# Performance work log

Hardware: AMD Instinct MI355X
Metric: run time of the kernel (lower is better)

## Reference

```python
import jax, jax.numpy as jnp
import numpy as np

NUM_HEADS = 12
WINDOW = 14
GLOBAL_LAYERS = (1,)
N_LAYERS = 2
EPS = 1e-6
PATCH = 16


def layer_norm(x, w, b):
    m = x.mean(-1, keepdims=True)
    v = ((x - m) ** 2).mean(-1, keepdims=True)
    return (x - m) * jax.lax.rsqrt(v + EPS) * w + b


def layer_norm_2d(x, w, b):
    # channels_first LayerNorm over C of [B,C,H,W]
    m = x.mean(1, keepdims=True)
    v = ((x - m) ** 2).mean(1, keepdims=True)
    return (x - m) * jax.lax.rsqrt(v + EPS) * w[None, :, None, None] + b[None, :, None, None]


def get_rel_pos(size, rel_pos):
    # q_size == k_size == size and rel_pos has exactly 2*size-1 rows,
    # so F.interpolate is identity -> direct relative-coordinate lookup.
    coords = jnp.arange(size)
    idx = coords[:, None] - coords[None, :] + (size - 1)  # [size, size]
    return rel_pos[idx]  # [size, size, head_dim]


def attention(x, qkv_w, qkv_b, proj_w, proj_b, rel_h, rel_w):
    B, H, W, C = x.shape
    hd = C // NUM_HEADS
    qkv = x.reshape(B, H * W, C) @ qkv_w.T + qkv_b                       # [B,HW,3C]
    qkv = qkv.reshape(B, H * W, 3, NUM_HEADS, hd).transpose(2, 0, 3, 1, 4)
    qkv = qkv.reshape(3, B * NUM_HEADS, H * W, hd)
    q, k, v = qkv[0], qkv[1], qkv[2]
    attn = jnp.einsum('bqd,bkd->bqk', q * (hd ** -0.5), k)               # [Bn,HW,HW]
    Rh = get_rel_pos(H, rel_h)                                           # [H,H,hd]
    Rw = get_rel_pos(W, rel_w)                                           # [W,W,hd]
    qr = q.reshape(B * NUM_HEADS, H, W, hd)
    rel_h_t = jnp.einsum('bhwc,hkc->bhwk', qr, Rh)                       # [Bn,H,W,H]
    rel_w_t = jnp.einsum('bhwc,wkc->bhwk', qr, Rw)                       # [Bn,H,W,W]
    attn = attn.reshape(B * NUM_HEADS, H, W, H, W)
    attn = attn + rel_h_t[:, :, :, :, None] + rel_w_t[:, :, :, None, :]
    attn = attn.reshape(B * NUM_HEADS, H * W, H * W)
    attn = jax.nn.softmax(attn.astype(jnp.float32), axis=-1).astype(q.dtype)
    out = jnp.einsum('bqk,bkd->bqd', attn, v)
    out = out.reshape(B, NUM_HEADS, H, W, hd).transpose(0, 2, 3, 1, 4).reshape(B, H, W, C)
    return out @ proj_w.T + proj_b


def window_partition(x, ws):
    B, H, W, C = x.shape
    pad_h = (-H) % ws
    pad_w = (-W) % ws
    x = jnp.pad(x, ((0, 0), (0, pad_h), (0, pad_w), (0, 0)))
    Hp, Wp = H + pad_h, W + pad_w
    x = x.reshape(B, Hp // ws, ws, Wp // ws, ws, C).transpose(0, 1, 3, 2, 4, 5)
    return x.reshape(-1, ws, ws, C), (Hp, Wp)


def window_unpartition(win, ws, pad_hw, hw):
    Hp, Wp = pad_hw
    H, W = hw
    C = win.shape[-1]
    B = win.shape[0] // ((Hp // ws) * (Wp // ws))
    x = win.reshape(B, Hp // ws, Wp // ws, ws, ws, C).transpose(0, 1, 3, 2, 4, 5)
    return x.reshape(B, Hp, Wp, C)[:, :H, :W, :]


def _forward(pixel_values, patch_w, patch_b, pos_embed, ln1_w, ln1_b, qkv_w, qkv_b,
             proj_w, proj_b, rel_h0, rel_w0, rel_h1, rel_w1, ln2_w, ln2_b,
             mlp1_w, mlp1_b, mlp2_w, mlp2_b, neck_conv1_w, neck_ln1_w, neck_ln1_b,
             neck_conv2_w, neck_ln2_w, neck_ln2_b):
    # patch embed (16x16 stride-16 conv) -> [B,64,64,768]
    x = jax.lax.conv_general_dilated(pixel_values, patch_w, (PATCH, PATCH), 'VALID',
                                     dimension_numbers=('NCHW', 'OIHW', 'NCHW'))
    x = x.transpose(0, 2, 3, 1) + patch_b
    x = x + pos_embed
    rels = [(rel_h0, rel_w0), (rel_h1, rel_w1)]
    for i in range(N_LAYERS):
        shortcut = x
        h = layer_norm(x, ln1_w[i], ln1_b[i])
        ws = 0 if i in GLOBAL_LAYERS else WINDOW
        if ws > 0:
            H, W = h.shape[1], h.shape[2]
            h, pad_hw = window_partition(h, ws)
        h = attention(h, qkv_w[i], qkv_b[i], proj_w[i], proj_b[i], *rels[i])
        if ws > 0:
            h = window_unpartition(h, ws, pad_hw, (H, W))
        x = shortcut + h
        m = layer_norm(x, ln2_w[i], ln2_b[i])
        m = jax.nn.gelu(m @ mlp1_w[i].T + mlp1_b[i], approximate=False)
        x = x + (m @ mlp2_w[i].T + mlp2_b[i])
    # neck: 1x1 conv -> LN2d -> 3x3 conv -> LN2d (convs have no bias)
    x = x.transpose(0, 3, 1, 2)                                          # [B,C,H,W]
    x = jnp.einsum('bchw,oc->bohw', x, neck_conv1_w[:, :, 0, 0])
    x = layer_norm_2d(x, neck_ln1_w, neck_ln1_b)
    x = jax.lax.conv_general_dilated(x, neck_conv2_w, (1, 1), ((1, 1), (1, 1)),
                                     dimension_numbers=('NCHW', 'OIHW', 'NCHW'))
    x = layer_norm_2d(x, neck_ln2_w, neck_ln2_b)
    return x


def setup_inputs() -> dict:
    ks = iter(jax.random.split(jax.random.key(0), 40))

    def rn(shape, s=0.02):
        return jax.random.normal(next(ks), shape, jnp.float32) * s

    C, NL, MLP, OC = 768, N_LAYERS, 3072, 256
    return {
        'pixel_values': jax.random.normal(next(ks), (1, 3, 1024, 1024), jnp.float32),
        'patch_w': rn((C, 3, PATCH, PATCH)),
        'patch_b': rn((C,)),
        'pos_embed': rn((1, 64, 64, C)),
        'ln1_w': jnp.ones((NL, C)), 'ln1_b': jnp.zeros((NL, C)),
        'qkv_w': rn((NL, 3 * C, C)), 'qkv_b': rn((NL, 3 * C)),
        'proj_w': rn((NL, C, C)), 'proj_b': rn((NL, C)),
        'rel_h0': rn((2 * WINDOW - 1, 64)), 'rel_w0': rn((2 * WINDOW - 1, 64)),
        'rel_h1': rn((2 * 64 - 1, 64)), 'rel_w1': rn((2 * 64 - 1, 64)),
        'ln2_w': jnp.ones((NL, C)), 'ln2_b': jnp.zeros((NL, C)),
        'mlp1_w': rn((NL, MLP, C)), 'mlp1_b': rn((NL, MLP)),
        'mlp2_w': rn((NL, C, MLP)), 'mlp2_b': rn((NL, C)),
        'neck_conv1_w': rn((OC, C, 1, 1)),
        'neck_ln1_w': jnp.ones((OC,)), 'neck_ln1_b': jnp.zeros((OC,)),
        'neck_conv2_w': rn((OC, OC, 3, 3)),
        'neck_ln2_w': jnp.ones((OC,)), 'neck_ln2_b': jnp.zeros((OC,)),
    }


def reference(pixel_values, patch_w, patch_b, pos_embed, ln1_w, ln1_b, qkv_w, qkv_b,
              proj_w, proj_b, rel_h0, rel_w0, rel_h1, rel_w1, ln2_w, ln2_b,
              mlp1_w, mlp1_b, mlp2_w, mlp2_b, neck_conv1_w, neck_ln1_w, neck_ln1_b,
              neck_conv2_w, neck_ln2_w, neck_ln2_b):
    return _forward(pixel_values, patch_w, patch_b, pos_embed, ln1_w, ln1_b, qkv_w,
                    qkv_b, proj_w, proj_b, rel_h0, rel_w0, rel_h1, rel_w1, ln2_w,
                    ln2_b, mlp1_w, mlp1_b, mlp2_w, mlp2_b, neck_conv1_w, neck_ln1_w,
                    neck_ln1_b, neck_conv2_w, neck_ln2_w, neck_ln2_b)
```

## Files before the change

kernel.cpp:

```cpp
#include <hip/hip_runtime.h>
#include <hip/hip_bf16.h>
#include <cmath>
#include <cstddef>

#define THREADS 256
typedef unsigned short u16;
typedef unsigned int u32;
typedef __attribute__((ext_vector_type(8))) short bf16x8;
typedef __attribute__((ext_vector_type(4))) float f32x4;
#define MFMA16(a, b, c) __builtin_amdgcn_mfma_f32_16x16x32_bf16(a, b, c, 0, 0, 0)

__device__ __forceinline__ float bf2f(u16 u) {
  union { u32 i; float f; } x; x.i = ((u32)u) << 16; return x.f;
}
__device__ __forceinline__ u16 f2bf(float f) {
  __hip_bfloat16 h = __float2bfloat16(f);
  return *reinterpret_cast<u16*>(&h);
}
__device__ __forceinline__ u32 f2bf2(float a, float b) {
  __hip_bfloat162 h = __float22bfloat162_rn(make_float2(a, b));
  return *reinterpret_cast<u32*>(&h);
}

__device__ __forceinline__ void gload16(const u16* g, u16* l) {
  __builtin_amdgcn_global_load_lds(
      (const __attribute__((address_space(1))) unsigned int*)g,
      (__attribute__((address_space(3))) unsigned int*)l, 16, 0, 0);
}

__device__ __forceinline__ float block_reduce_sum256(float v, float* red4) {
  for (int off = 32; off > 0; off >>= 1) v += __shfl_down(v, off);
  __syncthreads();
  if ((threadIdx.x & 63) == 0) red4[threadIdx.x >> 6] = v;
  __syncthreads();
  return red4[0] + red4[1] + red4[2] + red4[3];
}

__global__ void f2b_kernel(const float* __restrict__ in, u16* __restrict__ out,
                           int n) {
  int i = (blockIdx.x * THREADS + threadIdx.x) * 4;
  if (i >= n) return;
  float4 v = *reinterpret_cast<const float4*>(in + i);
  ushort4 o;
  o.x = f2bf(v.x); o.y = f2bf(v.y); o.z = f2bf(v.z); o.w = f2bf(v.w);
  *reinterpret_cast<ushort4*>(out + i) = o;
}

__global__ void neck2w_kernel(const float* __restrict__ src,
                              u16* __restrict__ dst) {
  int idx = blockIdx.x * THREADS + threadIdx.x;
  if (idx >= 256 * 2304) return;
  int o = idx / 2304, r = idx % 2304;
  int n9 = r >> 8, c = r & 255;
  dst[idx] = f2bf(src[(size_t)(o * 256 + c) * 9 + n9]);
}

__global__ void im2col_patch_kernel(const float* __restrict__ img,
                                    u16* __restrict__ out) {
  int idx = blockIdx.x * THREADS + threadIdx.x;
  if (idx >= 4096 * 768) return;
  int col = idx % 768, tok = idx / 768;
  int ph = tok / 64, pw = tok % 64;
  int c = col / 256, r = col % 256;
  int i = r / 16, j = r % 16;
  out[idx] = f2bf(img[(size_t)(c * 1024 + ph * 16 + i) * 1024 + pw * 16 + j]);
}

template <int MODE, int BN>
__global__ __launch_bounds__(256)
void gemm_bf16(const u16* __restrict__ A, const u16* __restrict__ B,
               const float* __restrict__ bias, const float* __restrict__ res,
               void* __restrict__ out, void* __restrict__ out2,
               int M, int N, int K) {
  constexpr int NF = BN / 32;
  __shared__ __attribute__((aligned(16))) u16 As[128 * 64];
  __shared__ __attribute__((aligned(16))) u16 Bs[BN * 64];
  const int t = threadIdx.x;
  const int w = t >> 6, l = t & 63;
  const int m0 = blockIdx.y * 128, n0 = blockIdx.x * BN;
  const int wm = (w >> 1) * 64, wn = (w & 1) * (BN / 2);
  f32x4 acc[4][NF];
#pragma unroll
  for (int i = 0; i < 4; ++i)
#pragma unroll
    for (int j = 0; j < NF; ++j) acc[i][j] = (f32x4){0.f, 0.f, 0.f, 0.f};

  const int rr = l >> 3;
  const int cc = ((l & 7) ^ rr) * 8;
  const u16* aP[4];
  const u16* bP[NF];
#pragma unroll
  for (int j = 0; j < 4; ++j) {
    int ar = m0 + w * 32 + j * 8 + rr;
    if (ar >= M) ar = M - 1;
    aP[j] = A + (size_t)ar * K + cc;
  }
#pragma unroll
  for (int j = 0; j < NF; ++j)
    bP[j] = B + (size_t)(n0 + w * (BN / 4) + j * 8 + rr) * K + cc;
  u16* asw = &As[w * 2048];
  u16* bsw = &Bs[w * (BN * 16)];

  for (int k0 = 0; k0 < K; k0 += 64) {
    __syncthreads();
#pragma unroll
    for (int j = 0; j < 4; ++j) gload16(aP[j] + k0, asw + j * 512);
#pragma unroll
    for (int j = 0; j < NF; ++j) gload16(bP[j] + k0, bsw + j * 512);
    asm volatile("s_waitcnt vmcnt(0)" ::: "memory");
    __syncthreads();
#pragma unroll
    for (int kc = 0; kc < 2; ++kc) {
      bf16x8 af[4], bf[NF];
#pragma unroll
      for (int i = 0; i < 4; ++i) {
        int ar = wm + i * 16 + (l & 15);
        int ac = (kc * 4 + (l >> 4)) ^ (ar & 7);
        af[i] = *reinterpret_cast<const bf16x8*>(&As[ar * 64 + ac * 8]);
      }
#pragma unroll
      for (int j = 0; j < NF; ++j) {
        int br = wn + j * 16 + (l & 15);
        int bc = (kc * 4 + (l >> 4)) ^ (br & 7);
        bf[j] = *reinterpret_cast<const bf16x8*>(&Bs[br * 64 + bc * 8]);
      }
#pragma unroll
      for (int i = 0; i < 4; ++i)
#pragma unroll
        for (int j = 0; j < NF; ++j)
          acc[i][j] = MFMA16(af[i], bf[j], acc[i][j]);
    }
  }

#pragma unroll
  for (int i = 0; i < 4; ++i) {
#pragma unroll
    for (int reg = 0; reg < 4; ++reg) {
      int m = m0 + wm + i * 16 + (l >> 4) * 4 + reg;
      if (m >= M) continue;
#pragma unroll
      for (int j = 0; j < NF; ++j) {
        int n = n0 + wn + j * 16 + (l & 15);
        float v = acc[i][j][reg];
        if (bias) v += bias[n];
        if (MODE == 0 || MODE == 3) {
          if (res) v += res[(size_t)m * N + n];
          ((float*)out)[(size_t)m * N + n] = v;
          if (MODE == 3) ((u16*)out2)[(size_t)m * N + n] = f2bf(v);
        } else if (MODE == 1) {
          v = 0.5f * v * (1.0f + erff(v * 0.70710678118654752f));
          ((u16*)out)[(size_t)m * N + n] = f2bf(v);
        } else {
          float sc = (n < 768) ? 0.125f : 1.0f;
          ((u16*)out)[(size_t)m * N + n] = f2bf(v * sc);
        }
      }
    }
  }
}

template <int WHICH>
__global__ __launch_bounds__(256)
void relpos_mfma_kernel(const u16* __restrict__ qkvb,
                        const u16* __restrict__ Rtab,
                        u16* __restrict__ relout) {
  __shared__ __attribute__((aligned(16))) u16 Ql[64 * 64];
  __shared__ __attribute__((aligned(16))) u16 Rl[64 * 64];
  const int t = threadIdx.x, w = t >> 6, l = t & 63;
  const int head = blockIdx.x >> 6;
  const int fixed = blockIdx.x & 63;
  const int rr = l >> 3;
  const int cc = ((l & 7) ^ rr) * 8;

#pragma unroll
  for (int j = 0; j < 2; ++j) {
    int row = w * 16 + j * 8 + rr;
    int tok = (WHICH == 0) ? (fixed * 64 + row) : (row * 64 + fixed);
    gload16(qkvb + (size_t)tok * 2304 + head * 64 + cc, &Ql[w * 1024 + j * 512]);
    int rrow = fixed - row + 63;
    gload16(Rtab + rrow * 64 + cc, &Rl[w * 1024 + j * 512]);
  }
  asm volatile("s_waitcnt vmcnt(0)" ::: "memory");
  __syncthreads();

  f32x4 acc[4];
#pragma unroll
  for (int j = 0; j < 4; ++j) acc[j] = (f32x4){0.f, 0.f, 0.f, 0.f};
#pragma unroll
  for (int kc = 0; kc < 2; ++kc) {
    int ar = w * 16 + (l & 15);
    int ac = (kc * 4 + (l >> 4)) ^ (ar & 7);
    bf16x8 af = *reinterpret_cast<const bf16x8*>(&Ql[ar * 64 + ac * 8]);
#pragma unroll
    for (int j = 0; j < 4; ++j) {
      int br = j * 16 + (l & 15);
      int bc = (kc * 4 + (l >> 4)) ^ (br & 7);
      bf16x8 bf = *reinterpret_cast<const bf16x8*>(&Rl[br * 64 + bc * 8]);
      acc[j] = MFMA16(af, bf, acc[j]);
    }
  }

#pragma unroll
  for (int j = 0; j < 4; ++j) {
#pragma unroll
    for (int reg = 0; reg < 4; ++reg) {
      int m = w * 16 + (l >> 4) * 4 + reg;
      int n = j * 16 + (l & 15);
      size_t o = (WHICH == 0)
                     ? ((((size_t)head * 64 + fixed) * 64 + m) * 64 + n)
                     : ((((size_t)head * 64 + m) * 64 + fixed) * 64 + n);
      relout[o] = f2bf(acc[j][reg] * 8.0f);
    }
  }
}

__global__ void ln_row_kernel(const float* __restrict__ in,
                              const float* __restrict__ w,
                              const float* __restrict__ b,
                              u16* __restrict__ out, int D) {
  __shared__ float red[4];
  size_t base = (size_t)blockIdx.x * D;
  float s = 0.f, s2 = 0.f;
  for (int i = threadIdx.x; i < D; i += THREADS) {
    float v = in[base + i];
    s += v; s2 += v * v;
  }
  s = block_reduce_sum256(s, red);
  s2 = block_reduce_sum256(s2, red);
  float m = s / (float)D;
  float var = s2 / (float)D - m * m;
  float inv = rsqrtf(var + 1e-6f);
  for (int i = threadIdx.x; i < D; i += THREADS) {
    float v = in[base + i];
    out[base + i] = f2bf((v - m) * inv * w[i] + b[i]);
  }
}

__global__ void win_part_kernel(const u16* __restrict__ h,
                                u16* __restrict__ out) {
  int idx = blockIdx.x * THREADS + threadIdx.x;
  if (idx >= 4900 * 768) return;
  int c = idx % 768;
  int tok = idx / 768;
  int win = tok / 196, r = tok % 196;
  int wy = r / 14, wx = r % 14;
  int gy = (win / 5) * 14 + wy;
  int gx = (win % 5) * 14 + wx;
  out[idx] = (gy < 64 && gx < 64) ? h[((size_t)gy * 64 + gx) * 768 + c] : (u16)0;
}

__global__ void win_unpart_add_kernel(const float* __restrict__ p,
                                      float* __restrict__ x) {
  int idx = blockIdx.x * THREADS + threadIdx.x;
  if (idx >= 4096 * 768) return;
  int c = idx % 768;
  int tok = idx / 768;
  int gy = tok / 64, gx = tok % 64;
  int win = (gy / 14) * 5 + (gx / 14);
  int wy = gy % 14, wx = gx % 14;
  x[idx] += p[((size_t)(win * 196 + wy * 14 + wx)) * 768 + c];
}

__global__ void add_kernel(const float* __restrict__ p, float* __restrict__ x,
                           int n) {
  int idx = blockIdx.x * THREADS + threadIdx.x;
  if (idx < n) x[idx] += p[idx];
}

__global__ void relpos_kernel(const u16* __restrict__ qkvb,
                              const float* __restrict__ rh_tab,
                              const float* __restrict__ rw_tab,
                              u16* __restrict__ relh,
                              u16* __restrict__ relw,
                              int S, int total) {
  int idx = blockIdx.x * THREADS + threadIdx.x;
  if (idx >= total) return;
  int k = idx % S;
  int r = idx / S;
  int qw = r % S; r /= S;
  int qh = r % S; r /= S;
  int head = r % 12;
  int win = r / 12;
  int seq = S * S;
  int tok = win * seq + qh * S + qw;
  const u16* q = qkvb + (size_t)tok * 2304 + head * 64;
  const float* rh = rh_tab + (size_t)(qh - k + S - 1) * 64;
  const float* rw = rw_tab + (size_t)(qw - k + S - 1) * 64;
  float sh = 0.f, sw = 0.f;
#pragma unroll
  for (int d0 = 0; d0 < 64; d0 += 8) {
    uint4 qv = *reinterpret_cast<const uint4*>(q + d0);
    u16 qs[8];
    *reinterpret_cast<uint4*>(qs) = qv;
#pragma unroll
    for (int i = 0; i < 8; ++i) {
      float qq = bf2f(qs[i]);
      sh = fmaf(qq, rh[d0 + i], sh);
      sw = fmaf(qq, rw[d0 + i], sw);
    }
  }
  relh[idx] = f2bf(sh * 8.0f);
  relw[idx] = f2bf(sw * 8.0f);
}

template <int S>
__global__ __launch_bounds__(256)
void attn_mfma_kernel(const u16* __restrict__ qkvb,
                      const u16* __restrict__ RHt,
                      const u16* __restrict__ RWt,
                      u16* __restrict__ out) {
  constexpr int SEQ = S * S;
  constexpr int NKT = (SEQ + 63) / 64;
  constexpr int BIAS_N = (S == 14) ? 320 : 1024;
  extern __shared__ __attribute__((aligned(16))) u16 smem[];
  u16* Kl = smem;
  u16* Vt = smem + 4096;
  u16* Plb = smem + 8192;
  u16* RHlb = smem + 12288;
  u16* RWlb = RHlb + 4 * BIAS_N;

  const int t = threadIdx.x;
  const int w = t >> 6;
  const int l = t & 63;
  const int g = l >> 4;
  const int q = l & 15;
  const int bn = blockIdx.y;
  const int win = bn / 12, head = bn % 12;
  const int qbase = blockIdx.x * 64 + w * 16;
  const size_t tokbase = (size_t)win * SEQ;
  u16* Pl = Plb + w * 1024;
  u16* RHl = RHlb + w * BIAS_N;
  u16* RWl = RWlb + w * BIAS_N;

  {
    int ql = l >> 2;
    int qglob = qbase + ql;
    if (qglob > SEQ - 1) qglob = SEQ - 1;
    int qh = qglob / S, qw = qglob - qh * S;
    size_t bh = (((size_t)bn * S + qh) * S + qw) * S;
    for (int i = l & 3; i < S; i += 4) {
      RHl[i * 16 + ql] = RHt[bh + i];
      if constexpr (S == 14) RWl[i * 16 + ql] = RWt[bh + i];
    }
  }

  float rwreg[4][4];
  if constexpr (S == 64) {
    int qglob = qbase + q;
    size_t rwb = (((size_t)bn * 64 + (qglob >> 6)) * 64 + (qglob & 63)) * 64;
#pragma unroll
    for (int sub = 0; sub < 4; ++sub)
#pragma unroll
      for (int reg = 0; reg < 4; ++reg)
        rwreg[sub][reg] = bf2f(RWt[rwb + sub * 16 + g * 4 + reg]);
  }

  bf16x8 qf[2];
  {
    int qglob = qbase + q;
    if (qglob > SEQ - 1) qglob = SEQ - 1;
    const u16* qp = qkvb + (tokbase + qglob) * 2304 + head * 64 + g * 8;
    qf[0] = *reinterpret_cast<const bf16x8*>(qp);
    qf[1] = *reinterpret_cast<const bf16x8*>(qp + 32);
  }

  float m_run = -1e30f, l_run = 0.f;
  f32x4 Oacc[4];
#pragma unroll
  for (int dn = 0; dn < 4; ++dn) Oacc[dn] = (f32x4){0.f, 0.f, 0.f, 0.f};

  const int rr = l >> 3;
  const int kcc = ((l & 7) ^ rr) * 8;

  for (int kt = 0; kt < NKT; ++kt) {
    const int k0 = kt * 64;
    __syncthreads();
    {
#pragma unroll
      for (int j = 0; j < 2; ++j) {
        int kk = k0 + w * 16 + j * 8 + rr;
        if (kk > SEQ - 1) kk = SEQ - 1;
        gload16(qkvb + (tokbase + kk) * 2304 + 768 + head * 64 + kcc,
                &Kl[w * 1024 + j * 512]);
      }
    }
    {
      int key = t & 63, dg = t >> 6;
      int kk = k0 + key; if (kk > SEQ - 1) kk = SEQ - 1;
      const uint4* src = reinterpret_cast<const uint4*>(
          qkvb + (tokbase + kk) * 2304 + 1536 + head * 64 + dg * 16);
      uint4 a = src[0], b = src[1];
      u16 arr[16];
      *reinterpret_cast<uint4*>(&arr[0]) = a;
      *reinterpret_cast<uint4*>(&arr[8]) = b;
#pragma unroll
      for (int i = 0; i < 16; ++i)
        Vt[(dg * 16 + i) * 64 + (key ^ ((i & 7) << 3))] = arr[i];
    }
    asm volatile("s_waitcnt vmcnt(0)" ::: "memory");
    __syncthreads();

    f32x4 Sacc[4];
#pragma unroll
    for (int sub = 0; sub < 4; ++sub) {
      Sacc[sub] = (f32x4){0.f, 0.f, 0.f, 0.f};
#pragma unroll
      for (int kc = 0; kc < 2; ++kc) {
        int key = sub * 16 + q;
        int chunk = (kc * 4 + g) ^ (key & 7);
        bf16x8 kfr = *reinterpret_cast<const bf16x8*>(&Kl[key * 64 + (chunk << 3)]);
        Sacc[sub] = MFMA16(kfr, qf[kc], Sacc[sub]);
      }
    }

    float sv[4][4];
    float tmax = -1e30f;
    if constexpr (S == 64) {
      float rhv = bf2f(RHl[kt * 16 + q]);
#pragma unroll
      for (int sub = 0; sub < 4; ++sub)
#pragma unroll
        for (int reg = 0; reg < 4; ++reg) {
          float s = Sacc[sub][reg] + rhv + rwreg[sub][reg];
          sv[sub][reg] = s;
          tmax = fmaxf(tmax, s);
        }
    } else {
#pragma unroll
      for (int sub = 0; sub < 4; ++sub)
#pragma unroll
        for (int reg = 0; reg < 4; ++reg) {
          int key = k0 + sub * 16 + g * 4 + reg;
          float s = -1e30f;
          if (key < SEQ) {
            int kh = key / S, kw = key - kh * S;
            s = Sacc[sub][reg] + bf2f(RHl[kh * 16 + q]) + bf2f(RWl[kw * 16 + q]);
          }
          sv[sub][reg] = s;
          tmax = fmaxf(tmax, s);
        }
    }
    tmax = fmaxf(tmax, __shfl_xor(tmax, 16));
    tmax = fmaxf(tmax, __shfl_xor(tmax, 32));

    if (!__all(tmax - m_run <= 8.0f)) {
      float mn = fmaxf(m_run, tmax);
      float sc = __expf(m_run - mn);
      l_run *= sc;
      m_run = mn;
#pragma unroll
      for (int reg = 0; reg < 4; ++reg) {
        float scq = __shfl(sc, g * 4 + reg);
#pragma unroll
        for (int dn = 0; dn < 4; ++dn) Oacc[dn][reg] *= scq;
      }
    }

    float psum = 0.f;
#pragma unroll
    for (int sub = 0; sub < 4; ++sub)
#pragma unroll
      for (int pr = 0; pr < 2; ++pr) {
        float p0 = __expf(sv[sub][2 * pr] - m_run);
        float p1 = __expf(sv[sub][2 * pr + 1] - m_run);
        psum += p0 + p1;
        u32 pk = f2bf2(p0, p1);
        int idx = (q * 64 + sub * 16 + g * 4 + pr * 2) ^ ((q & 7) << 3);
        *reinterpret_cast<u32*>(&Pl[idx]) = pk;
      }
    psum += __shfl_xor(psum, 16);
    psum += __shfl_xor(psum, 32);
    l_run += psum;

#pragma unroll
    for (int kc = 0; kc < 2; ++kc) {
      int chunk = (kc * 4 + g) ^ (q & 7);
      bf16x8 pa = *reinterpret_cast<const bf16x8*>(&Pl[q * 64 + (chunk << 3)]);
#pragma unroll
      for (int dn = 0; dn < 4; ++dn) {
        bf16x8 vb = *reinterpret_cast<const bf16x8*>(
            &Vt[(dn * 16 + q) * 64 + (chunk << 3)]);
        Oacc[dn] = MFMA16(pa, vb, Oacc[dn]);
      }
    }
  }

  float invq = 1.0f / l_run;
#pragma unroll
  for (int reg = 0; reg < 4; ++reg) {
    int ql = g * 4 + reg;
    int qglob = qbase + ql;
    if (qglob >= SEQ) continue;
    float inv = __shfl(invq, ql);
    u16* op = out + (tokbase + qglob) * 768 + head * 64;
#pragma unroll
    for (int dn = 0; dn < 4; ++dn)
      op[dn * 16 + q] = f2bf(Oacc[dn][reg] * inv);
  }
}

__global__ void neck_im2col_kernel(const u16* __restrict__ ln,
                                   u16* __restrict__ out) {
  int idx = blockIdx.x * THREADS + threadIdx.x;
  if (idx >= 4096 * 2304) return;
  int col = idx % 2304, tok = idx / 2304;
  int n9 = col >> 8, c = col & 255;
  int y = tok >> 6, x = tok & 63;
  int yy = y + n9 / 3 - 1, xx = x + n9 % 3 - 1;
  out[idx] = (yy >= 0 && yy < 64 && xx >= 0 && xx < 64)
                 ? ln[((size_t)yy * 64 + xx) * 256 + c]
                 : (u16)0;
}

__global__ void ln2d_out_kernel(const float* __restrict__ in,
                                const float* __restrict__ w,
                                const float* __restrict__ b,
                                float* __restrict__ out) {
  __shared__ float red[4];
  int tok = blockIdx.x, t = threadIdx.x;
  float v = in[(size_t)tok * 256 + t];
  float s = block_reduce_sum256(v, red);
  float m = s / 256.f;
  float dv = v - m;
  float s2 = block_reduce_sum256(dv * dv, red);
  float inv = rsqrtf(s2 / 256.f + 1e-6f);
  out[(size_t)t * 4096 + tok] = dv * inv * w[t] + b[t];
}

extern "C" void kernel_launch(void* const* d_in, const int* in_sizes, int n_in,
                              void* d_out, int out_size, void* d_ws,
                              size_t ws_size, hipStream_t stream) {
  const float* pixel_values = (const float*)d_in[0];
  const float* patch_w = (const float*)d_in[1];
  const float* patch_b = (const float*)d_in[2];
  const float* pos_embed = (const float*)d_in[3];
  const float* ln1_w = (const float*)d_in[4];
  const float* ln1_b = (const float*)d_in[5];
  const float* qkv_w = (const float*)d_in[6];
  const float* qkv_b = (const float*)d_in[7];
  const float* proj_w = (const float*)d_in[8];
  const float* proj_b = (const float*)d_in[9];
  const float* rel_h0 = (const float*)d_in[10];
  const float* rel_w0 = (const float*)d_in[11];
  const float* rel_h1 = (const float*)d_in[12];
  const float* rel_w1 = (const float*)d_in[13];
  const float* ln2_w = (const float*)d_in[14];
  const float* ln2_b = (const float*)d_in[15];
  const float* mlp1_w = (const float*)d_in[16];
  const float* mlp1_b = (const float*)d_in[17];
  const float* mlp2_w = (const float*)d_in[18];
  const float* mlp2_b = (const float*)d_in[19];
  const float* neck1_w = (const float*)d_in[20];
  const float* nln1_w = (const float*)d_in[21];
  const float* nln1_b = (const float*)d_in[22];
  const float* neck2_w = (const float*)d_in[23];
  const float* nln2_w = (const float*)d_in[24];
  const float* nln2_b = (const float*)d_in[25];
  float* out = (float*)d_out;

  float* X = (float*)d_ws;
  u16* Xb = (u16*)(X + 3145728);
  float* H = (float*)(Xb + 3145728);
  u16* Ab1 = (u16*)(H + 3763200);
  u16* Ab2 = Ab1 + 3763200;
  u16* QKVb = Ab2 + 12582912;
  u16* RHb = QKVb + 11289600;
  u16* RWb = RHb + 3145728;
  u16* AOb = RWb + 3145728;
  u16* Wb = AOb + 3763200;
  u16* RTb = Wb + 2359296;
  u16* RTb2 = RTb + 8128;
  u16* LNb = Ab2 + 11520000;

#define CVT(src, n) f2b_kernel<<<((n) / 4 + THREADS - 1) / THREADS, THREADS, 0, stream>>>(src, Wb, n)

  im2col_patch_kernel<<<12288, THREADS, 0, stream>>>(pixel_values, Ab2);
  CVT(patch_w, 589824);
  gemm_bf16<0, 64><<<dim3(12, 32), THREADS, 0, stream>>>(
      Ab2, Wb, patch_b, pos_embed, X, nullptr, 4096, 768, 768);

  ln_row_kernel<<<4096, THREADS, 0, stream>>>(X, ln1_w, ln1_b, Ab2, 768);
  win_part_kernel<<<14700, THREADS, 0, stream>>>(Ab2, Ab1);
  CVT(qkv_w, 1769472);
  gemm_bf16<2, 128><<<dim3(18, 39), THREADS, 0, stream>>>(
      Ab1, Wb, qkv_b, nullptr, QKVb, nullptr, 4900, 2304, 768);
  {
    int total = 25 * 12 * 14 * 14 * 14;
    relpos_kernel<<<(total + THREADS - 1) / THREADS, THREADS, 0, stream>>>(
        QKVb, rel_h0, rel_w0, RHb, RWb, 14, total);
  }
  attn_mfma_kernel<14><<<dim3(4, 300), THREADS, 29696, stream>>>(QKVb, RHb, RWb, AOb);
  CVT(proj_w, 589824);
  gemm_bf16<0, 64><<<dim3(12, 39), THREADS, 0, stream>>>(
      AOb, Wb, proj_b, nullptr, H, nullptr, 4900, 768, 768);
  win_unpart_add_kernel<<<12288, THREADS, 0, stream>>>(H, X);
  ln_row_kernel<<<4096, THREADS, 0, stream>>>(X, ln2_w, ln2_b, Ab1, 768);
  CVT(mlp1_w, 2359296);
  gemm_bf16<1, 128><<<dim3(24, 32), THREADS, 0, stream>>>(
      Ab1, Wb, mlp1_b, nullptr, Ab2, nullptr, 4096, 3072, 768);
  CVT(mlp2_w, 2359296);
  gemm_bf16<0, 64><<<dim3(12, 32), THREADS, 0, stream>>>(
      Ab2, Wb, mlp2_b, X, X, nullptr, 4096, 768, 3072);

  ln_row_kernel<<<4096, THREADS, 0, stream>>>(X, ln1_w + 768, ln1_b + 768, Ab1, 768);
  CVT(qkv_w + (size_t)2304 * 768, 1769472);
  gemm_bf16<2, 128><<<dim3(18, 32), THREADS, 0, stream>>>(
      Ab1, Wb, qkv_b + 2304, nullptr, QKVb, nullptr, 4096, 2304, 768);
  f2b_kernel<<<8, THREADS, 0, stream>>>(rel_h1, RTb, 8128);
  f2b_kernel<<<8, THREADS, 0, stream>>>(rel_w1, RTb2, 8128);
  relpos_mfma_kernel<0><<<768, THREADS, 0, stream>>>(QKVb, RTb, RHb);
  relpos_mfma_kernel<1><<<768, THREADS, 0, stream>>>(QKVb, RTb2, RWb);
  attn_mfma_kernel<64><<<dim3(64, 12), THREADS, 32768, stream>>>(QKVb, RHb, RWb, AOb);
  CVT(proj_w + (size_t)768 * 768, 589824);
  gemm_bf16<0, 64><<<dim3(12, 32), THREADS, 0, stream>>>(
      AOb, Wb, proj_b + 768, nullptr, H, nullptr, 4096, 768, 768);
  add_kernel<<<12288, THREADS, 0, stream>>>(H, X, 4096 * 768);
  ln_row_kernel<<<4096, THREADS, 0, stream>>>(X, ln2_w + 768, ln2_b + 768, Ab1, 768);
  CVT(mlp1_w + (size_t)3072 * 768, 2359296);
  gemm_bf16<1, 128><<<dim3(24, 32), THREADS, 0, stream>>>(
      Ab1, Wb, mlp1_b + 3072, nullptr, Ab2, nullptr, 4096, 3072, 768);
  CVT(mlp2_w + (size_t)768 * 3072, 2359296);
  gemm_bf16<3, 64><<<dim3(12, 32), THREADS, 0, stream>>>(
      Ab2, Wb, mlp2_b + 768, X, X, Xb, 4096, 768, 3072);

  CVT(neck1_w, 196608);
  gemm_bf16<0, 64><<<dim3(4, 32), THREADS, 0, stream>>>(
      Xb, Wb, nullptr, nullptr, H, nullptr, 4096, 256, 768);
  ln_row_kernel<<<4096, THREADS, 0, stream>>>(H, nln1_w, nln1_b, LNb, 256);
  neck2w_kernel<<<2304, THREADS, 0, stream>>>(neck2_w, Wb);
  neck_im2col_kernel<<<36864, THREADS, 0, stream>>>(LNb, Ab2);
  gemm_bf16<0, 64><<<dim3(4, 32), THREADS, 0, stream>>>(
      Ab2, Wb, nullptr, nullptr, H, nullptr, 4096, 256, 2304);
  ln2d_out_kernel<<<4096, THREADS, 0, stream>>>(H, nln2_w, nln2_b, out);
}
```

Baseline: 996.3 us.

## Double-buffer K/V tiles in global attention kernel to overlap loads with compute

For the S=64 global-attention instantiation, K and V tiles now use two LDS buffers. The next tile's K async loads and V register loads are issued before computing the current tile, and V is written to LDS afterwards. This removes one barrier per iteration and hides global memory latency behind the MFMA work. In exchange, LDS use rises from 32KB to 48KB per block, which may lower occupancy, and V staging holds extra registers across the compute.

```diff
diff --git a/kernel.cpp b/kernel.cpp
--- a/kernel.cpp
+++ b/kernel.cpp
@@ -311,13 +311,26 @@
                       u16* __restrict__ out) {
   constexpr int SEQ = S * S;
   constexpr int NKT = (SEQ + 63) / 64;
+  constexpr bool DB = (S == 64);
   constexpr int BIAS_N = (S == 14) ? 320 : 1024;
   extern __shared__ __attribute__((aligned(16))) u16 smem[];
-  u16* Kl = smem;
-  u16* Vt = smem + 4096;
-  u16* Plb = smem + 8192;
-  u16* RHlb = smem + 12288;
-  u16* RWlb = RHlb + 4 * BIAS_N;
+  u16* KlA[2];
+  u16* VtA[2];
+  u16* Plb;
+  u16* RHlb;
+  u16* RWlb = nullptr;
+  if constexpr (DB) {
+    KlA[0] = smem;          KlA[1] = smem + 4096;
+    VtA[0] = smem + 8192;   VtA[1] = smem + 12288;
+    Plb = smem + 16384;
+    RHlb = smem + 20480;
+  } else {
+    KlA[0] = smem;          KlA[1] = smem;
+    VtA[0] = smem + 4096;   VtA[1] = smem + 4096;
+    Plb = smem + 8192;
+    RHlb = smem + 12288;
+    RWlb = RHlb + 4 * BIAS_N;
+  }
 
   const int t = threadIdx.x;
   const int w = t >> 6;
@@ -371,35 +384,36 @@
 
   const int rr = l >> 3;
   const int kcc = ((l & 7) ^ rr) * 8;
-
-  for (int kt = 0; kt < NKT; ++kt) {
+  const int vkey = t & 63, vdg = t >> 6;
+
+  auto stageK = [&](int kt, u16* Kd) {
+#pragma unroll
+    for (int j = 0; j < 2; ++j) {
+      int kk = kt * 64 + w * 16 + j * 8 + rr;
+      if (kk > SEQ - 1) kk = SEQ - 1;
+      gload16(qkvb + (tokbase + kk) * 2304 + 768 + head * 64 + kcc,
+              &Kd[w * 1024 + j * 512]);
+    }
+  };
+  auto loadV = [&](int kt, uint4& a, uint4& b) {
+    int kk = kt * 64 + vkey;
+    if (kk > SEQ - 1) kk = SEQ - 1;
+    const uint4* src = reinterpret_cast<const uint4*>(
+        qkvb + (tokbase + kk) * 2304 + 1536 + head * 64 + vdg * 16);
+    a = src[0];
+    b = src[1];
+  };
+  auto writeV = [&](uint4 a, uint4 b, u16* Vd) {
+    u16 arr[16];
+    *reinterpret_cast<uint4*>(&arr[0]) = a;
+    *reinterpret_cast<uint4*>(&arr[8]) = b;
+#pragma unroll
+    for (int i = 0; i < 16; ++i)
+      Vd[(vdg * 16 + i) * 64 + (vkey ^ ((i & 7) << 3))] = arr[i];
+  };
+
+  auto computeTile = [&](int kt, u16* Kl, u16* Vt) {
     const int k0 = kt * 64;
-    __syncthreads();
-    {
-#pragma unroll
-      for (int j = 0; j < 2; ++j) {
-        int kk = k0 + w * 16 + j * 8 + rr;
-        if (kk > SEQ - 1) kk = SEQ - 1;
-        gload16(qkvb + (tokbase + kk) * 2304 + 768 + head * 64 + kcc,
-                &Kl[w * 1024 + j * 512]);
-      }
-    }
-    {
-      int key = t & 63, dg = t >> 6;
-      int kk = k0 + key; if (kk > SEQ - 1) kk = SEQ - 1;
-      const uint4* src = reinterpret_cast<const uint4*>(
-          qkvb + (tokbase + kk) * 2304 + 1536 + head * 64 + dg * 16);
-      uint4 a = src[0], b = src[1];
-      u16 arr[16];
-      *reinterpret_cast<uint4*>(&arr[0]) = a;
-      *reinterpret_cast<uint4*>(&arr[8]) = b;
-#pragma unroll
-      for (int i = 0; i < 16; ++i)
-        Vt[(dg * 16 + i) * 64 + (key ^ ((i & 7) << 3))] = arr[i];
-    }
-    asm volatile("s_waitcnt vmcnt(0)" ::: "memory");
-    __syncthreads();
-
     f32x4 Sacc[4];
 #pragma unroll
     for (int sub = 0; sub < 4; ++sub) {
@@ -482,6 +496,40 @@
             &Vt[(dn * 16 + q) * 64 + (chunk << 3)]);
         Oacc[dn] = MFMA16(pa, vb, Oacc[dn]);
       }
+    }
+  };
+
+  if constexpr (DB) {
+    uint4 va, vb0;
+    stageK(0, KlA[0]);
+    loadV(0, va, vb0);
+    asm volatile("s_waitcnt vmcnt(0)" ::: "memory");
+    writeV(va, vb0, VtA[0]);
+    __syncthreads();
+    for (int kt = 0; kt < NKT; ++kt) {
+      const int cur = kt & 1;
+      const bool pf = (kt + 1 < NKT);
+      if (pf) {
+        stageK(kt + 1, KlA[cur ^ 1]);
+        loadV(kt + 1, va, vb0);
+      }
+      computeTile(kt, KlA[cur], VtA[cur]);
+      if (pf) {
+        asm volatile("s_waitcnt vmcnt(0)" ::: "memory");
+        writeV(va, vb0, VtA[cur ^ 1]);
+      }
+      __syncthreads();
+    }
+  } else {
+    for (int kt = 0; kt < NKT; ++kt) {
+      __syncthreads();
+      stageK(kt, KlA[0]);
+      uint4 va, vb0;
+      loadV(kt, va, vb0);
+      writeV(va, vb0, VtA[0]);
+      asm volatile("s_waitcnt vmcnt(0)" ::: "memory");
+      __syncthreads();
+      computeTile(kt, KlA[0], VtA[0]);
     }
   }
 
@@ -610,7 +658,7 @@
   f2b_kernel<<<8, THREADS, 0, stream>>>(rel_w1, RTb2, 8128);
   relpos_mfma_kernel<0><<<768, THREADS, 0, stream>>>(QKVb, RTb, RHb);
   relpos_mfma_kernel<1><<<768, THREADS, 0, stream>>>(QKVb, RTb2, RWb);
-  attn_mfma_kernel<64><<<dim3(64, 12), THREADS, 32768, stream>>>(QKVb, RHb, RWb, AOb);
+  attn_mfma_kernel<64><<<dim3(64, 12), THREADS, 49152, stream>>>(QKVb, RHb, RWb, AOb);
   CVT(proj_w + (size_t)768 * 768, 589824);
   gemm_bf16<0, 64><<<dim3(12, 32), THREADS, 0, stream>>>(
       AOb, Wb, proj_b + 768, nullptr, H, nullptr, 4096, 768, 768);
```

Result: slower. 1.030 ms (+3.4%).
